# Performance work log

Measured on AMD Instinct MI355X. Metric: run time of the kernel, lower is better.

Reference implementation:

```python
import jax, jax.numpy as jnp
import numpy as np

B, N, C = 4, 2048, 64   # batch, tokens, num_feat
HS = 512                # hidden_size
H = HS // C             # 8 heads, head_dim = C = 64
EPS = 1e-6


def _ln(x, g, b):
    m = x.mean(-1, keepdims=True)
    v = ((x - m) ** 2).mean(-1, keepdims=True)
    return (x - m) / jnp.sqrt(v + EPS) * g + b


def setup_inputs() -> dict:
    key = jax.random.key(0)
    ks = jax.random.split(key, 8)
    s = 0.02
    return {
        "x": jax.random.normal(ks[0], (B, N, C), jnp.float32),
        "g1": jnp.ones((C,), jnp.float32),
        "be1": jnp.zeros((C,), jnp.float32),
        "Wqkv": jax.random.normal(ks[1], (C, 3 * HS), jnp.float32) * s,
        "bqkv": jnp.zeros((3 * HS,), jnp.float32),
        "Wout": jax.random.normal(ks[2], (HS, C), jnp.float32) * s,
        "bout": jnp.zeros((C,), jnp.float32),
        "g2": jnp.ones((C,), jnp.float32),
        "be2": jnp.zeros((C,), jnp.float32),
        "W1": jax.random.normal(ks[3], (C, HS // 8), jnp.float32) * s,
        "b1": jax.random.normal(ks[4], (HS // 8,), jnp.float32) * 1e-6,
        "W2": jax.random.normal(ks[5], (HS // 8, C), jnp.float32) * s,
        "b2": jax.random.normal(ks[6], (C,), jnp.float32) * 1e-6,
    }


def reference(x, g1, be1, Wqkv, bqkv, Wout, bout, g2, be2, W1, b1, W2, b2):
    b_, n_, c_ = x.shape
    hs = Wout.shape[0]
    h_ = hs // c_
    res = x
    y = _ln(x, g1, be1)
    # fused QKV: (B,N,3*HS) -> (3,B,H,N,D) with D = c_
    qkv = (y @ Wqkv + bqkv).reshape(b_, n_, 3, h_, c_).transpose(2, 0, 3, 1, 4)
    q, k, v = qkv[0], qkv[1], qkv[2]
    scores = jnp.einsum('bhqd,bhkd->bhqk', q, k) / jnp.sqrt(jnp.asarray(c_, x.dtype))
    probs = jax.nn.softmax(scores, axis=-1)
    ctx = jnp.einsum('bhqk,bhkd->bhqd', probs, v)
    ctx = ctx.transpose(0, 2, 1, 3).reshape(b_, n_, hs)
    attn = jax.nn.gelu(ctx @ Wout + bout, approximate=False)  # GELU after out proj per source
    x2 = attn + res
    y2 = _ln(x2, g2, be2)
    mlp = jax.nn.gelu(y2 @ W1 + b1, approximate=False) @ W2 + b2
    return mlp + x2
```

## Files before the change

kernel.cpp:

```cpp
#include <hip/hip_runtime.h>


#define NN 2048
#define CC 64
#define HH 8
#define HSZ 512
#define QKSCALE 0.42466092f

typedef __bf16 bf16x8 __attribute__((ext_vector_type(8)));
typedef float f32x4 __attribute__((ext_vector_type(4)));

__device__ __forceinline__ float b2f(unsigned short u) {
  union { unsigned int i; float f; } v; v.i = ((unsigned int)u) << 16; return v.f;
}
__device__ __forceinline__ unsigned short f2b(float f) {
  union { float f; unsigned int i; } v; v.f = f;
  unsigned int r = v.i + 0x7FFFu + ((v.i >> 16) & 1u);
  return (unsigned short)(r >> 16);
}
__device__ __forceinline__ unsigned int pk2(float a, float b) {
  return (unsigned int)f2b(a) | ((unsigned int)f2b(b) << 16);
}
__device__ __forceinline__ unsigned char f2fp8(float f) {
  int p = __builtin_amdgcn_cvt_pk_fp8_f32(f, f, 0, false);
  return (unsigned char)(p & 0xFF);
}
__device__ __forceinline__ float gelu_f(float x) {
  return 0.5f * x * (1.0f + erff(x * 0.7071067811865475f));
}

__global__ __launch_bounds__(256) void k_ln_qkv(
    const float* __restrict__ x,
    const float* __restrict__ g1,
    const float* __restrict__ be1,
    const float* __restrict__ W,
    const float* __restrict__ bqkv,
    unsigned char* __restrict__ Qb,
    unsigned char* __restrict__ Kb,
    unsigned char* __restrict__ VbT)
{
  __shared__ __align__(16) unsigned short As[64 * 72];
  __shared__ __align__(16) unsigned short Ws[128 * 72];
  unsigned char* Es = (unsigned char*)As;
  const int tid = threadIdx.x, wv = tid >> 6, lane = tid & 63;
  const int col = lane & 15, quad = lane >> 4;
  const int bm = blockIdx.x & 127, bn = blockIdx.x >> 7;
  const int m0 = bm * 64, nw = bn * 128;

  const int c4 = tid & 15;
  float4 gv = *(const float4*)(g1 + c4 * 4);
  float4 bv = *(const float4*)(be1 + c4 * 4);
  #pragma unroll
  for (int s = 0; s < 4; ++s) {
    int idx = s * 256 + tid;
    int row = idx >> 4;
    float4 xv = *(const float4*)(x + (size_t)(m0 + row) * CC + c4 * 4);
    float ps = xv.x + xv.y + xv.z + xv.w;
    float ps2 = xv.x * xv.x + xv.y * xv.y + xv.z * xv.z + xv.w * xv.w;
    #pragma unroll
    for (int off = 8; off; off >>= 1) {
      ps += __shfl_xor(ps, off, 16);
      ps2 += __shfl_xor(ps2, off, 16);
    }
    float mean = ps * (1.0f / 64.0f);
    float var = ps2 * (1.0f / 64.0f) - mean * mean;
    float rs = rsqrtf(var + 1e-6f);
    uint2 packed;
    packed.x = pk2((xv.x - mean) * rs * gv.x + bv.x, (xv.y - mean) * rs * gv.y + bv.y);
    packed.y = pk2((xv.z - mean) * rs * gv.z + bv.z, (xv.w - mean) * rs * gv.w + bv.w);
    *(uint2*)&As[row * 72 + c4 * 4] = packed;
  }

  {
    const int c_loc = tid & 127;
    const int kg = tid >> 7;
    const int ng = nw + c_loc;
    #pragma unroll
    for (int g = 0; g < 4; ++g) {
      float wv8[8];
      #pragma unroll
      for (int j = 0; j < 8; ++j) wv8[j] = W[(size_t)(kg * 32 + g * 8 + j) * 1536 + ng];
      uint4 u;
      u.x = pk2(wv8[0], wv8[1]); u.y = pk2(wv8[2], wv8[3]);
      u.z = pk2(wv8[4], wv8[5]); u.w = pk2(wv8[6], wv8[7]);
      *(uint4*)&Ws[c_loc * 72 + kg * 32 + g * 8] = u;
    }
  }
  __syncthreads();

  bf16x8 af0 = *(const bf16x8*)&As[(wv * 16 + col) * 72 + quad * 8];
  bf16x8 af1 = *(const bf16x8*)&As[(wv * 16 + col) * 72 + 32 + quad * 8];

  f32x4 acc[8];
  #pragma unroll
  for (int nt = 0; nt < 8; ++nt) acc[nt] = (f32x4){0.f, 0.f, 0.f, 0.f};
  #pragma unroll
  for (int nt = 0; nt < 8; ++nt) {
    bf16x8 b0 = *(const bf16x8*)&Ws[(nt * 16 + col) * 72 + quad * 8];
    bf16x8 b1 = *(const bf16x8*)&Ws[(nt * 16 + col) * 72 + 32 + quad * 8];
    acc[nt] = __builtin_amdgcn_mfma_f32_16x16x32_bf16(af0, b0, acc[nt], 0, 0, 0);
    acc[nt] = __builtin_amdgcn_mfma_f32_16x16x32_bf16(af1, b1, acc[nt], 0, 0, 0);
  }
  __syncthreads();

  const int bb = m0 >> 11;
  const int nloc = m0 & 2047;
  const int which = nw >> 9;
  const int hbase = (nw >> 6) & 7;
  const int tloc = wv * 16 + quad * 4;

  if (which == 2) {
    #pragma unroll
    for (int nt = 0; nt < 8; ++nt) {
      const int hb = nt >> 2, d0 = (nt & 3) * 16;
      const float bias = bqkv[nw + nt * 16 + col];
      int lo = __builtin_amdgcn_cvt_pk_fp8_f32(acc[nt][0] + bias, acc[nt][1] + bias, 0, false);
      int full = __builtin_amdgcn_cvt_pk_fp8_f32(acc[nt][2] + bias, acc[nt][3] + bias, lo, true);
      *(unsigned int*)&Es[hb * 4096 + (d0 + col) * 64 + tloc] = (unsigned int)full;
    }
    __syncthreads();
    const int d = tid >> 2, nseg = (tid & 3) * 16;
    #pragma unroll
    for (int hb = 0; hb < 2; ++hb) {
      size_t off = ((size_t)(bb * HH + hbase + hb) * CC + d) * NN + nloc + nseg;
      *(uint4*)(VbT + off) = *(const uint4*)&Es[hb * 4096 + tid * 16];
    }
  } else {
    const float scale = (which == 0) ? QKSCALE : 1.0f;
    #pragma unroll
    for (int nt = 0; nt < 8; ++nt) {
      const int hb = nt >> 2, d0 = (nt & 3) * 16;
      const float bias = bqkv[nw + nt * 16 + col];
      #pragma unroll
      for (int r = 0; r < 4; ++r)
        Es[hb * 4096 + (tloc + r) * 64 + d0 + col] = f2fp8((acc[nt][r] + bias) * scale);
    }
    __syncthreads();
    unsigned char* dst = (which == 0) ? Qb : Kb;
    #pragma unroll
    for (int hb = 0; hb < 2; ++hb) {
      size_t off = ((size_t)(bb * HH + hbase + hb) * NN + nloc) * CC + tid * 16;
      *(uint4*)(dst + off) = *(const uint4*)&Es[hb * 4096 + tid * 16];
    }
  }
}

__global__ __launch_bounds__(256) void k_attn(
    const unsigned char* __restrict__ Q,
    const unsigned char* __restrict__ K,
    const unsigned char* __restrict__ VT,
    const float* __restrict__ Wout,
    unsigned short* __restrict__ part,
    float* __restrict__ lsums)
{
  __shared__ __align__(16) unsigned char smem[27648];
  unsigned short* Wb = (unsigned short*)smem;
  unsigned short* Ob = (unsigned short*)(smem + 9216);
  const int tid = threadIdx.x, wv = tid >> 6, lane = tid & 63;
  const int col = lane & 15, quad = lane >> 4;
  const int bid = blockIdx.x;
  const int tc = bid & 1, qc = (bid >> 1) & 15, bh = bid >> 5;
  const size_t base = (size_t)bh * NN * CC;
  const int q0 = qc * 128 + wv * 32;
  const int t0 = tc * 1024;
  const int srow = tid >> 2, sc16 = (tid & 3) << 4;

  if (tid < 160) {
    int bsel = tid >= 80, t2 = tid - bsel * 80;
    unsigned int fill = (t2 < 5) ? 0x38383838u : 0u;
    uint4 u; u.x = fill; u.y = fill; u.z = fill; u.w = fill;
    *(uint4*)&smem[bsel * 11520 + 5120 + 64 * 80 + t2 * 16] = u;
  }

  long qf[2][2];
  #pragma unroll
  for (int mt = 0; mt < 2; ++mt)
    #pragma unroll
    for (int kh = 0; kh < 2; ++kh)
      qf[mt][kh] = *(const long*)(Q + base + (size_t)(q0 + mt * 16 + col) * CC + kh * 32 + quad * 8);

  f32x4 o[2][4];
  f32x4 ol[2];
  #pragma unroll
  for (int mt = 0; mt < 2; ++mt) {
    #pragma unroll
    for (int dt = 0; dt < 4; ++dt) o[mt][dt] = (f32x4){0.f, 0.f, 0.f, 0.f};
    ol[mt] = (f32x4){0.f, 0.f, 0.f, 0.f};
  }
  const int sl0 = ((quad & 1) << 5) + col;
  const int sl1 = sl0 + 16;
  const bool hiq = (quad >= 2);

  {
    *(uint4*)&smem[srow * 80 + sc16] =
        *(const uint4*)(K + base + (size_t)(t0 + srow) * CC + sc16);
    *(uint4*)&smem[5120 + srow * 80 + sc16] =
        *(const uint4*)(VT + base + (size_t)srow * NN + t0 + sc16);
  }
  __syncthreads();

  for (int kt = 0; kt < 16; ++kt) {
    unsigned char* Ks = smem + (kt & 1) * 11520;
    unsigned char* Vt = Ks + 5120;
    uint4 kreg, vreg;
    const bool more = (kt + 1) < 16;
    if (more) {
      const int tb2 = t0 + (kt + 1) * 64;
      kreg = *(const uint4*)(K + base + (size_t)(tb2 + srow) * CC + sc16);
      vreg = *(const uint4*)(VT + base + (size_t)srow * NN + tb2 + sc16);
    }

    unsigned int Dw[2][4];
    #pragma unroll
    for (int ct = 0; ct < 4; ++ct) {
      long k0 = *(const long*)&Ks[(ct * 16 + col) * 80 + quad * 8];
      long k1 = *(const long*)&Ks[(ct * 16 + col) * 80 + 32 + quad * 8];
      #pragma unroll
      for (int mt = 0; mt < 2; ++mt) {
        f32x4 a = (f32x4){0.f, 0.f, 0.f, 0.f};
        a = __builtin_amdgcn_mfma_f32_16x16x32_fp8_fp8(k0, qf[mt][0], a, 0, 0, 0);
        a = __builtin_amdgcn_mfma_f32_16x16x32_fp8_fp8(k1, qf[mt][1], a, 0, 0, 0);
        float p0 = __builtin_amdgcn_exp2f(a[0]);
        float p1 = __builtin_amdgcn_exp2f(a[1]);
        float p2 = __builtin_amdgcn_exp2f(a[2]);
        float p3 = __builtin_amdgcn_exp2f(a[3]);
        int lo = __builtin_amdgcn_cvt_pk_fp8_f32(p0, p1, 0, false);
        Dw[mt][ct] = (unsigned int)__builtin_amdgcn_cvt_pk_fp8_f32(p2, p3, lo, true);
      }
    }

    #pragma unroll
    for (int kh = 0; kh < 2; ++kh) {
      long pb[2];
      #pragma unroll
      for (int mt = 0; mt < 2; ++mt) {
        unsigned int a0 = (unsigned int)__shfl((int)Dw[mt][2 * kh], sl0, 64);
        unsigned int b0 = (unsigned int)__shfl((int)Dw[mt][2 * kh + 1], sl0, 64);
        unsigned int a1 = (unsigned int)__shfl((int)Dw[mt][2 * kh], sl1, 64);
        unsigned int b1 = (unsigned int)__shfl((int)Dw[mt][2 * kh + 1], sl1, 64);
        unsigned long lo = hiq ? b0 : a0;
        unsigned long hi = hiq ? b1 : a1;
        pb[mt] = (long)(lo | (hi << 32));
      }
      #pragma unroll
      for (int dt = 0; dt < 4; ++dt) {
        long vf = *(const long*)&Vt[(dt * 16 + col) * 80 + kh * 32 + quad * 8];
        o[0][dt] = __builtin_amdgcn_mfma_f32_16x16x32_fp8_fp8(vf, pb[0], o[0][dt], 0, 0, 0);
        o[1][dt] = __builtin_amdgcn_mfma_f32_16x16x32_fp8_fp8(vf, pb[1], o[1][dt], 0, 0, 0);
      }
      long vl = *(const long*)&Vt[(64 + col) * 80 + kh * 32 + quad * 8];
      ol[0] = __builtin_amdgcn_mfma_f32_16x16x32_fp8_fp8(vl, pb[0], ol[0], 0, 0, 0);
      ol[1] = __builtin_amdgcn_mfma_f32_16x16x32_fp8_fp8(vl, pb[1], ol[1], 0, 0, 0);
    }

    if (more) {
      unsigned char* Kn = smem + ((kt + 1) & 1) * 11520;
      *(uint4*)&Kn[srow * 80 + sc16] = kreg;
      *(uint4*)&Kn[5120 + srow * 80 + sc16] = vreg;
    }
    __syncthreads();
  }

  const int h = bh & 7, b = bh >> 3;
  #pragma unroll
  for (int mt = 0; mt < 2; ++mt) {
    if (quad == 0)
      lsums[(size_t)(tc * 32 + bh) * NN + q0 + mt * 16 + col] = ol[mt][0];
  }

  {
    const int c = tid & 63, kg = tid >> 6;
    #pragma unroll
    for (int j = 0; j < 16; ++j)
      Wb[c * 72 + kg * 16 + j] = f2b(Wout[(size_t)(h * 64 + kg * 16 + j) * 64 + c]);
  }
  unsigned short* Obw = Ob + wv * (32 * 72);
  #pragma unroll
  for (int mt = 0; mt < 2; ++mt)
    #pragma unroll
    for (int dt = 0; dt < 4; ++dt) {
      uint2 u;
      u.x = pk2(o[mt][dt][0], o[mt][dt][1]);
      u.y = pk2(o[mt][dt][2], o[mt][dt][3]);
      *(uint2*)&Obw[(mt * 16 + col) * 72 + dt * 16 + quad * 4] = u;
    }
  __syncthreads();

  #pragma unroll
  for (int mt = 0; mt < 2; ++mt) {
    bf16x8 oa0 = *(const bf16x8*)&Obw[(mt * 16 + col) * 72 + quad * 8];
    bf16x8 oa1 = *(const bf16x8*)&Obw[(mt * 16 + col) * 72 + 32 + quad * 8];
    #pragma unroll
    for (int nt = 0; nt < 4; ++nt) {
      bf16x8 bw0 = *(const bf16x8*)&Wb[(nt * 16 + col) * 72 + quad * 8];
      bf16x8 bw1 = *(const bf16x8*)&Wb[(nt * 16 + col) * 72 + 32 + quad * 8];
      f32x4 ac = (f32x4){0.f, 0.f, 0.f, 0.f};
      ac = __builtin_amdgcn_mfma_f32_16x16x32_bf16(oa0, bw0, ac, 0, 0, 0);
      ac = __builtin_amdgcn_mfma_f32_16x16x32_bf16(oa1, bw1, ac, 0, 0, 0);
      #pragma unroll
      for (int r = 0; r < 4; ++r) {
        int n = q0 + mt * 16 + quad * 4 + r;
        part[((size_t)(tc * 32 + bh) * NN + n) * CC + nt * 16 + col] = f2b(ac[r]);
      }
    }
  }
}

__global__ __launch_bounds__(256) void k_post(
    const unsigned short* __restrict__ part,
    const float* __restrict__ lsums,
    const float* __restrict__ x,
    const float* __restrict__ bout,
    const float* __restrict__ g2,
    const float* __restrict__ be2,
    const float* __restrict__ W1,
    const float* __restrict__ b1,
    const float* __restrict__ W2,
    const float* __restrict__ b2v,
    float* __restrict__ out)
{
  __shared__ __align__(16) unsigned short Ws1[64 * 64];
  __shared__ __align__(16) unsigned short Ws2[64 * 64];
  __shared__ float ys[8][64], hs[8][64];
  const int tid = threadIdx.x, wid = tid >> 6, lane = tid & 63;
  const int w2 = wid * 2;
  const int tk0 = blockIdx.x * 8 + w2;

  #pragma unroll
  for (int p = 0; p < 4; ++p) {
    int idx = p * 256 + tid;
    float4 a1 = *(const float4*)(W1 + idx * 4);
    float4 a2 = *(const float4*)(W2 + idx * 4);
    uint2 u1; u1.x = pk2(a1.x, a1.y); u1.y = pk2(a1.z, a1.w);
    uint2 u2; u2.x = pk2(a2.x, a2.y); u2.y = pk2(a2.z, a2.w);
    *(uint2*)&Ws1[idx * 4] = u1;
    *(uint2*)&Ws2[idx * 4] = u2;
  }

  const float boutl = bout[lane];
  const float g2l = g2[lane], be2l = be2[lane];
  float x2v[2];
  #pragma unroll
  for (int t = 0; t < 2; ++t) {
    const int tk = tk0 + t;
    const int b = tk >> 11, n = tk & 2047;
    float proj = 0.f;
    #pragma unroll
    for (int h = 0; h < 8; ++h) {
      size_t i0 = (size_t)(b * HH + h) * NN + n;
      size_t i1 = i0 + (size_t)32 * NN;
      float p = b2f(part[i0 * CC + lane]) + b2f(part[i1 * CC + lane]);
      float l = lsums[i0] + lsums[i1];
      proj += p * __builtin_amdgcn_rcpf(l);
    }
    float a = gelu_f(proj + boutl);
    float x2 = a + x[(size_t)tk * CC + lane];
    x2v[t] = x2;
    float s = x2;
    #pragma unroll
    for (int off = 32; off; off >>= 1) s += __shfl_xor(s, off, 64);
    float mean = s * (1.0f / 64.0f);
    float d = x2 - mean;
    float vs = d * d;
    #pragma unroll
    for (int off = 32; off; off >>= 1) vs += __shfl_xor(vs, off, 64);
    float var = vs * (1.0f / 64.0f);
    ys[w2 + t][lane] = d * rsqrtf(var + 1e-6f) * g2l + be2l;
  }
  __syncthreads();

  float acc2[2] = {0.f, 0.f};
  #pragma unroll 8
  for (int c = 0; c < 64; ++c) {
    float w = b2f(Ws1[c * 64 + lane]);
    acc2[0] += ys[w2][c] * w;
    acc2[1] += ys[w2 + 1][c] * w;
  }
  const float b1l = b1[lane];
  hs[w2][lane] = gelu_f(acc2[0] + b1l);
  hs[w2 + 1][lane] = gelu_f(acc2[1] + b1l);

  float acc3[2] = {0.f, 0.f};
  #pragma unroll 8
  for (int c = 0; c < 64; ++c) {
    float w = b2f(Ws2[c * 64 + lane]);
    acc3[0] += hs[w2][c] * w;
    acc3[1] += hs[w2 + 1][c] * w;
  }
  const float b2l = b2v[lane];
  #pragma unroll
  for (int t = 0; t < 2; ++t)
    out[(size_t)(tk0 + t) * CC + lane] = acc3[t] + b2l + x2v[t];
}

extern "C" void kernel_launch(void* const* d_in, const int* in_sizes, int n_in,
                              void* d_out, int out_size, void* d_ws, size_t ws_size,
                              hipStream_t stream) {
  const float* x    = (const float*)d_in[0];
  const float* g1   = (const float*)d_in[1];
  const float* be1  = (const float*)d_in[2];
  const float* Wqkv = (const float*)d_in[3];
  const float* bqkv = (const float*)d_in[4];
  const float* Wout = (const float*)d_in[5];
  const float* bout = (const float*)d_in[6];
  const float* g2   = (const float*)d_in[7];
  const float* be2  = (const float*)d_in[8];
  const float* W1   = (const float*)d_in[9];
  const float* b1   = (const float*)d_in[10];
  const float* W2   = (const float*)d_in[11];
  const float* b2   = (const float*)d_in[12];
  float* out = (float*)d_out;

  unsigned char* wsb = (unsigned char*)d_ws;
  const size_t SZ = (size_t)4 * HH * NN * CC;
  unsigned char* Qb   = wsb;
  unsigned char* Kb   = wsb + SZ;
  unsigned char* VbT  = wsb + 2 * SZ;
  unsigned short* part = (unsigned short*)(wsb + 3 * SZ);
  float* lsums         = (float*)(wsb + 3 * SZ + 4 * SZ);

  k_ln_qkv<<<1536, 256, 0, stream>>>(x, g1, be1, Wqkv, bqkv, Qb, Kb, VbT);
  k_attn<<<1024, 256, 0, stream>>>(Qb, Kb, VbT, Wout, part, lsums);
  k_post<<<1024, 256, 0, stream>>>(part, lsums, x, bout, g2, be2, W1, b1, W2, b2, out);
}
```

Before: 152.6 us.

## Single-buffer K/V tiles in attention with padded 88-byte LDS row stride

Replaces the double-buffered K/V shared-memory tiles, whose next tile was prefetched into registers, with a single buffer that is loaded and synchronised at the start of each iteration. The row stride changes from 80 to 88 bytes to alter the LDS bank mapping. The ones-row used for row sums is now written at the new offsets. This drops the register prefetch and half the LDS footprint, but global load latency is no longer hidden behind compute and each iteration gains a barrier. The init code also contains a leftover odd fill loop.

```diff
diff --git a/kernel.cpp b/kernel.cpp
--- a/kernel.cpp
+++ b/kernel.cpp
@@ -6,6 +6,7 @@
 #define HH 8
 #define HSZ 512
 #define QKSCALE 0.42466092f
+#define LSTR 88
 
 typedef __bf16 bf16x8 __attribute__((ext_vector_type(8)));
 typedef float f32x4 __attribute__((ext_vector_type(4)));
@@ -154,6 +155,8 @@
     float* __restrict__ lsums)
 {
   __shared__ __align__(16) unsigned char smem[27648];
+  unsigned char* Ks = smem;
+  unsigned char* Vt = smem + 5632;
   unsigned short* Wb = (unsigned short*)smem;
   unsigned short* Ob = (unsigned short*)(smem + 9216);
   const int tid = threadIdx.x, wv = tid >> 6, lane = tid & 63;
@@ -165,12 +168,21 @@
   const int t0 = tc * 1024;
   const int srow = tid >> 2, sc16 = (tid & 3) << 4;
 
-  if (tid < 160) {
-    int bsel = tid >= 80, t2 = tid - bsel * 80;
-    unsigned int fill = (t2 < 5) ? 0x38383838u : 0u;
-    uint4 u; u.x = fill; u.y = fill; u.z = fill; u.w = fill;
-    *(uint4*)&smem[bsel * 11520 + 5120 + 64 * 80 + t2 * 16] = u;
-  }
+  if (tid < 80) {
+    unsigned int fill = (tid == 0) ? 0x38383838u : 0u;
+    #pragma unroll
+    for (int w8 = 0; w8 < 11; ++w8)
+      *(unsigned int*)&Vt[(64 + (tid >> 0) % 16) * LSTR + 0] = 0u;
+  }
+  {
+    int idx = tid * 8;
+    if (idx < 16 * LSTR) {
+      unsigned long long z = 0ull;
+      *(unsigned long long*)&Vt[64 * LSTR + idx] = z;
+    }
+  }
+  __syncthreads();
+  if (tid < 11) *(unsigned int*)&Vt[64 * LSTR + tid * 4] = 0x38383838u;
 
   long qf[2][2];
   #pragma unroll
@@ -191,30 +203,23 @@
   const int sl1 = sl0 + 16;
   const bool hiq = (quad >= 2);
 
-  {
-    *(uint4*)&smem[srow * 80 + sc16] =
-        *(const uint4*)(K + base + (size_t)(t0 + srow) * CC + sc16);
-    *(uint4*)&smem[5120 + srow * 80 + sc16] =
-        *(const uint4*)(VT + base + (size_t)srow * NN + t0 + sc16);
-  }
-  __syncthreads();
-
   for (int kt = 0; kt < 16; ++kt) {
-    unsigned char* Ks = smem + (kt & 1) * 11520;
-    unsigned char* Vt = Ks + 5120;
-    uint4 kreg, vreg;
-    const bool more = (kt + 1) < 16;
-    if (more) {
-      const int tb2 = t0 + (kt + 1) * 64;
-      kreg = *(const uint4*)(K + base + (size_t)(tb2 + srow) * CC + sc16);
-      vreg = *(const uint4*)(VT + base + (size_t)srow * NN + tb2 + sc16);
-    }
+    const int tb = t0 + kt * 64;
+    {
+      uint4 kv = *(const uint4*)(K + base + (size_t)(tb + srow) * CC + sc16);
+      uint4 vv = *(const uint4*)(VT + base + (size_t)srow * NN + tb + sc16);
+      *(uint2*)&Ks[srow * LSTR + sc16] = make_uint2(kv.x, kv.y);
+      *(uint2*)&Ks[srow * LSTR + sc16 + 8] = make_uint2(kv.z, kv.w);
+      *(uint2*)&Vt[srow * LSTR + sc16] = make_uint2(vv.x, vv.y);
+      *(uint2*)&Vt[srow * LSTR + sc16 + 8] = make_uint2(vv.z, vv.w);
+    }
+    __syncthreads();
 
     unsigned int Dw[2][4];
     #pragma unroll
     for (int ct = 0; ct < 4; ++ct) {
-      long k0 = *(const long*)&Ks[(ct * 16 + col) * 80 + quad * 8];
-      long k1 = *(const long*)&Ks[(ct * 16 + col) * 80 + 32 + quad * 8];
+      long k0 = *(const long*)&Ks[(ct * 16 + col) * LSTR + quad * 8];
+      long k1 = *(const long*)&Ks[(ct * 16 + col) * LSTR + 32 + quad * 8];
       #pragma unroll
       for (int mt = 0; mt < 2; ++mt) {
         f32x4 a = (f32x4){0.f, 0.f, 0.f, 0.f};
@@ -244,19 +249,13 @@
       }
       #pragma unroll
       for (int dt = 0; dt < 4; ++dt) {
-        long vf = *(const long*)&Vt[(dt * 16 + col) * 80 + kh * 32 + quad * 8];
+        long vf = *(const long*)&Vt[(dt * 16 + col) * LSTR + kh * 32 + quad * 8];
         o[0][dt] = __builtin_amdgcn_mfma_f32_16x16x32_fp8_fp8(vf, pb[0], o[0][dt], 0, 0, 0);
         o[1][dt] = __builtin_amdgcn_mfma_f32_16x16x32_fp8_fp8(vf, pb[1], o[1][dt], 0, 0, 0);
       }
-      long vl = *(const long*)&Vt[(64 + col) * 80 + kh * 32 + quad * 8];
+      long vl = *(const long*)&Vt[(64 + col) * LSTR + kh * 32 + quad * 8];
       ol[0] = __builtin_amdgcn_mfma_f32_16x16x32_fp8_fp8(vl, pb[0], ol[0], 0, 0, 0);
       ol[1] = __builtin_amdgcn_mfma_f32_16x16x32_fp8_fp8(vl, pb[1], ol[1], 0, 0, 0);
-    }
-
-    if (more) {
-      unsigned char* Kn = smem + ((kt + 1) & 1) * 11520;
-      *(uint4*)&Kn[srow * 80 + sc16] = kreg;
-      *(uint4*)&Kn[5120 + srow * 80 + sc16] = vreg;
     }
     __syncthreads();
   }
```

Result: faster. 147.3 us (-3.5%).
